# Optimization experiments

Measured on AMD Instinct MI355X. Metric: run time of the kernel, lower is better.

Reference implementation:

```python
import jax, jax.numpy as jnp
import numpy as np

N, F_IN, H, C, E = 50000, 128, 4, 32, 800000
NEG_SLOPE = 0.2


def setup_inputs() -> dict:
    key = jax.random.key(0)
    ks = jax.random.split(key, 6)
    x = jax.random.normal(ks[0], (N, F_IN), dtype=jnp.float32)
    edge_index = jax.random.randint(ks[1], (2, E), 0, N, dtype=jnp.int64)
    scale = 1.0 / np.sqrt(F_IN)
    Wl = jax.random.normal(ks[2], (F_IN, H * C), dtype=jnp.float32) * scale
    Wr = jax.random.normal(ks[3], (F_IN, H * C), dtype=jnp.float32) * scale
    att = jax.random.normal(ks[4], (H, C), dtype=jnp.float32) * (1.0 / np.sqrt(C))
    bias = jax.random.normal(ks[5], (H * C,), dtype=jnp.float32) * 0.01
    return {"x": x, "edge_index": edge_index, "Wl": Wl, "Wr": Wr, "att": att, "bias": bias}


def reference(x, edge_index, Wl, Wr, att, bias):
    n = x.shape[0]
    # add self loops (add_self_loops=True, edge_dim=None)
    loop = jnp.arange(n, dtype=edge_index.dtype)
    ei = jnp.concatenate([edge_index, jnp.stack([loop, loop])], axis=1)
    src, dst = ei[0], ei[1]  # messages flow src -> dst; softmax over dst
    # share_weights=False: separate projections for source (l) and target (r)
    xl = (x @ Wl).reshape(n, H, C)
    xr = (x @ Wr).reshape(n, H, C)
    # GATv2 edge score: a . LeakyReLU(xl[src] + xr[dst])
    e = xl[src] + xr[dst]                      # [Et, H, C]
    e = jnp.where(e > 0, e, NEG_SLOPE * e)
    logits = jnp.einsum('ehc,hc->eh', e, att)  # [Et, H]
    # segment softmax over destination nodes (every node has a self loop)
    m = jax.ops.segment_max(logits, dst, num_segments=n)
    ex = jnp.exp(logits - m[dst])
    den = jax.ops.segment_sum(ex, dst, num_segments=n)
    alpha = ex / den[dst]                      # [Et, H]
    # weighted scatter-aggregate of source messages
    out = jax.ops.segment_sum(alpha[:, :, None] * xl[src], dst, num_segments=n)
    out = out.reshape(n, H * C) + bias         # concat=True heads, bias
    out = jax.nn.relu(out)                     # activation_func='relu'
    return out, alpha
```

## Files before the change

### kernel.cpp

```cpp
#include <hip/hip_runtime.h>
#include <hip/hip_bf16.h>
#include <hip/hip_fp16.h>

#define F_IN   128
#define HC     128
#define NH     4
#define NEG_SLOPE 0.2f
#define CAP    5120

typedef __attribute__((ext_vector_type(8))) short short8;
typedef __attribute__((ext_vector_type(4))) float f32x4;
typedef _Float16 h2 __attribute__((ext_vector_type(2)));

__device__ __forceinline__ unsigned short f2bf(float f) {
    union { float f; unsigned u; } c; c.f = f;
    unsigned u = c.u;
    u += 0x7FFFu + ((u >> 16) & 1u);
    return (unsigned short)(u >> 16);
}

__device__ __forceinline__ float fdot2f(h2 a, h2 b, float c) {
#if __has_builtin(__builtin_amdgcn_fdot2)
    return __builtin_amdgcn_fdot2(a, b, c, false);
#else
    return fmaf((float)a[0], (float)b[0], fmaf((float)a[1], (float)b[1], c));
#endif
}

union U4H { uint4 u; h2 h[4]; };

__global__ __launch_bounds__(256) void wpack_zero_kernel(
    const float* __restrict__ Wl, const float* __restrict__ Wr,
    short* __restrict__ BlP, short* __restrict__ BrP,
    int* __restrict__ bucketCount)
{
    if ((int)blockIdx.x >= 16) {
        bucketCount[threadIdx.x] = 0;
        return;
    }
    const int tid = blockIdx.x * 256 + threadIdx.x;
    const int mat = tid >> 11;
    const int r   = tid & 2047;
    const int f   = r >> 6;
    const int l   = r & 63;
    const int t   = f & 3;
    const int ct  = f >> 2;
    const int kb  = t * 32 + (l >> 4) * 8;
    const int c   = ct * 16 + (l & 15);
    const float* W = mat ? Wr : Wl;
    short*       P = mat ? BrP : BlP;
    short8 v;
    #pragma unroll
    for (int j = 0; j < 8; ++j)
        v[j] = (short)f2bf(W[(size_t)(kb + j) * HC + c]);
    *(short8*)&P[(size_t)(f * 64 + l) * 8] = v;
}

__global__ __launch_bounds__(1024) void proj_split_kernel(
    const float* __restrict__ x,
    const short* __restrict__ BlP,
    const short* __restrict__ BrP,
    unsigned short* __restrict__ xlb,
    unsigned short* __restrict__ xrb,
    const int* __restrict__ ei,
    int* __restrict__ bucketCount,
    int2* __restrict__ slotES,
    int n, int E, int PB, int NB)
{
    __shared__ int sA[256];
    __shared__ int sB[256];
    const int t = threadIdx.x;

    if ((int)blockIdx.x >= PB) {
        const int e0 = ((int)blockIdx.x - PB) * 4096;

        if (t < 256) sA[t] = 0;
        __syncthreads();
        int dsts[4], srcs[4];
        #pragma unroll
        for (int k = 0; k < 4; ++k) {
            const int e = e0 + k * 1024 + t;
            dsts[k] = (e < E) ? ei[E + e] : -1;
            srcs[k] = (e < E) ? ei[e] : 0;
        }
        #pragma unroll
        for (int k = 0; k < 4; ++k)
            if (dsts[k] >= 0) atomicAdd(&sA[dsts[k] >> 8], 1);
        __syncthreads();
        if (t < NB) sB[t] = atomicAdd(&bucketCount[t], sA[t]);
        __syncthreads();
        if (t < 256) sA[t] = 0;
        __syncthreads();
        #pragma unroll
        for (int k = 0; k < 4; ++k) {
            const int e = e0 + k * 1024 + t;
            if (dsts[k] >= 0) {
                const int b = dsts[k] >> 8;
                const int r = sB[b] + atomicAdd(&sA[b], 1);
                slotES[(size_t)b * CAP + r] =
                    make_int2(e | ((dsts[k] & 255) << 24), srcs[k]);
            }
        }
        return;
    }

    const int w    = t >> 6;
    const int lane = t & 63;
    const int r0   = blockIdx.x * 256 + w * 16;
    if (r0 >= n) return;
    const int q    = lane >> 4;
    const int row  = r0 + (lane & 15);

    short8 af[4];
    {
        const float* xp = x + (size_t)row * F_IN + q * 8;
        #pragma unroll
        for (int s = 0; s < 4; ++s) {
            const float4 u0 = *(const float4*)(xp + s * 32);
            const float4 u1 = *(const float4*)(xp + s * 32 + 4);
            short8 a;
            a[0] = (short)f2bf(u0.x); a[1] = (short)f2bf(u0.y);
            a[2] = (short)f2bf(u0.z); a[3] = (short)f2bf(u0.w);
            a[4] = (short)f2bf(u1.x); a[5] = (short)f2bf(u1.y);
            a[6] = (short)f2bf(u1.z); a[7] = (short)f2bf(u1.w);
            af[s] = a;
        }
    }

    f32x4 accL[8], accR[8];
    const f32x4 zero = {0.f, 0.f, 0.f, 0.f};
    #pragma unroll
    for (int ct = 0; ct < 8; ++ct) { accL[ct] = zero; accR[ct] = zero; }

    #pragma unroll
    for (int s = 0; s < 4; ++s) {
        #pragma unroll
        for (int ct = 0; ct < 8; ++ct) {
            const short8 bl = *(const short8*)&BlP[(size_t)((ct * 4 + s) * 64 + lane) * 8];
            const short8 br = *(const short8*)&BrP[(size_t)((ct * 4 + s) * 64 + lane) * 8];
            accL[ct] = __builtin_amdgcn_mfma_f32_16x16x32_bf16(af[s], bl, accL[ct], 0, 0, 0);
            accR[ct] = __builtin_amdgcn_mfma_f32_16x16x32_bf16(af[s], br, accR[ct], 0, 0, 0);
        }
    }

    const int cb = lane & 15;
    const bool evenLane = (cb & 1) == 0;
    unsigned* xl_u = (unsigned*)xlb;
    unsigned* xr_u = (unsigned*)xrb;
    #pragma unroll
    for (int ct = 0; ct < 8; ++ct) {
        #pragma unroll
        for (int i = 0; i < 4; ++i) {
            const float l = accL[ct][i];
            const float r = accR[ct][i];
            const float sl = __shfl_xor(l, 1);
            const float sr = __shfl_xor(r, 1);
            const int rowo = r0 + q * 4 + i;
            const size_t cidx = (size_t)rowo * 64 + ct * 8 + (cb >> 1);
            union { _Float16 h[2]; unsigned u; } ph;
            if (evenLane) { ph.h[0] = (_Float16)l;  ph.h[1] = (_Float16)sl; xl_u[cidx] = ph.u; }
            else          { ph.h[0] = (_Float16)sr; ph.h[1] = (_Float16)r;  xr_u[cidx] = ph.u; }
        }
    }
}

__global__ __launch_bounds__(1024) void bucket_build_kernel(
    const int* __restrict__ bucketCount,
    const int2* __restrict__ slotES,
    int* __restrict__ rowptr,
    int2* __restrict__ csr,
    int n, int E, int NB)
{
    __shared__ int sh[256];
    __shared__ int cur[256];
    const int t = threadIdx.x;
    const int b = blockIdx.x;

    if (t < 256) sh[t] = (t < NB) ? bucketCount[t] : 0;
    __syncthreads();
    for (int off = 1; off < 256; off <<= 1) {
        int v = 0, u = 0;
        if (t < 256) { v = sh[t]; u = (t >= off) ? sh[t - off] : 0; }
        __syncthreads();
        if (t < 256) sh[t] = v + u;
        __syncthreads();
    }
    const int base = (b == 0) ? 0 : sh[b - 1];
    const int cnt  = sh[b] - base;
    __syncthreads();

    if (t < 256) cur[t] = 0;
    __syncthreads();
    const size_t sbase = (size_t)b * CAP;
    int2 rec[5]; int nrec = 0;
    for (int i = t; i < cnt; i += 1024) {
        rec[nrec] = slotES[sbase + i];
        ++nrec;
    }
    for (int k = 0; k < nrec; ++k)
        atomicAdd(&cur[(unsigned)rec[k].x >> 24], 1);
    __syncthreads();

    int myCnt = 0;
    if (t < 256) { myCnt = cur[t]; sh[t] = myCnt; }
    __syncthreads();
    for (int off = 1; off < 256; off <<= 1) {
        int v = 0, u = 0;
        if (t < 256) { v = sh[t]; u = (t >= off) ? sh[t - off] : 0; }
        __syncthreads();
        if (t < 256) sh[t] = v + u;
        __syncthreads();
    }
    if (t < 256) {
        const int startT = sh[t] - myCnt;
        const int dstT = (b << 8) + t;
        if (dstT < n) rowptr[dstT] = base + startT;
        if (b == 0 && t == 0) rowptr[n] = E;
        cur[t] = startT;
    }
    __syncthreads();

    for (int k = 0; k < nrec; ++k) {
        const int dl = (unsigned)rec[k].x >> 24;
        const int r = atomicAdd(&cur[dl], 1);
        csr[(size_t)base + r] = make_int2(rec[k].x & 0xFFFFFF, rec[k].y);
    }
}

__global__ __launch_bounds__(256) void fused_agg_kernel(
    const int2* __restrict__ csr,
    const int* __restrict__ rowptr,
    const unsigned short* __restrict__ xlb,
    const unsigned short* __restrict__ xrb,
    const float* __restrict__ att,
    const float* __restrict__ bias,
    float* __restrict__ alpha_out,
    float* __restrict__ out,
    int n, int E)
{
    __shared__ float lds_ex[4][256];
    const int w    = threadIdx.x >> 6;
    const int lane = threadIdx.x & 63;
    const int dst  = blockIdx.x * 4 + w;
    if (dst >= n) return;

    const int start = rowptr[dst];
    const int deg   = rowptr[dst + 1] - start;
    const int total = deg + 1;
    const int g     = lane >> 4;
    const int i     = lane & 15;
    const int h     = i >> 2;

    const uint4* xl_u = (const uint4*)xlb;

    h2 xr2[4], at2[4];
    {
        U4H c; c.u = ((const uint4*)xrb)[(size_t)dst * 16 + i];
        xr2[0] = c.h[0]; xr2[1] = c.h[1]; xr2[2] = c.h[2]; xr2[3] = c.h[3];
        const float4 a01 = *(const float4*)&att[8 * i];
        const float4 a23 = *(const float4*)&att[8 * i + 4];
        at2[0] = h2{(_Float16)a01.x, (_Float16)a01.y};
        at2[1] = h2{(_Float16)a01.z, (_Float16)a01.w};
        at2[2] = h2{(_Float16)a23.x, (_Float16)a23.y};
        at2[3] = h2{(_Float16)a23.z, (_Float16)a23.w};
    }
    const h2 slope2 = {(_Float16)NEG_SLOPE, (_Float16)NEG_SLOPE};

    int eReg = E + dst, srcReg = dst;
    if (lane < deg) { const int2 es = csr[start + lane]; eReg = es.x; srcReg = es.y; }

    float* exrow = lds_ex[w];

    float dh = 0.f;
    float acc[8];
    #pragma unroll
    for (int k = 0; k < 8; ++k) acc[k] = 0.f;

    int j = 0;
    {
        const int s0 = __shfl(srcReg, g);
        uint4 u = xl_u[(size_t)s0 * 16 + i];
        uint4 u1 = u;
        if (4 < total) {
            const int s1 = __shfl(srcReg, min(g + 4, 63));
            u1 = xl_u[(size_t)s1 * 16 + i];
        }

        for (; j < total && j <= 60; j += 4) {
            const int jj = j + g;
            uint4 u2 = u1;
            if (j + 8 < total) {
                const int sn = __shfl(srcReg, min(jj + 8, 63));
                u2 = xl_u[(size_t)sn * 16 + i];
            }

            U4H cu; cu.u = u;
            float p = 0.f;
            float vf[8];
            #pragma unroll
            for (int k = 0; k < 4; ++k) {
                const h2 v2 = cu.h[k];
                const h2 t2 = v2 + xr2[k];
                const h2 l2 = __builtin_elementwise_max(t2, t2 * slope2);
                p = fdot2f(l2, at2[k], p);
                vf[2 * k]     = (float)v2[0];
                vf[2 * k + 1] = (float)v2[1];
            }
            p += __shfl_xor(p, 1);
            p += __shfl_xor(p, 2);

            const float ex = (jj <= deg) ? __expf(p) : 0.f;
            dh += ex;
            #pragma unroll
            for (int k = 0; k < 8; ++k) acc[k] = fmaf(ex, vf[k], acc[k]);

            if ((lane & 3) == 0 && jj <= deg) exrow[jj * 4 + h] = ex;
            u = u1; u1 = u2;
        }
    }
    for (; j < total; j += 4) {
        const int jj = j + g;
        const int cidx = start + min(jj, deg - 1);
        const int2 es = csr[cidx];
        const int s   = (jj < deg) ? es.y : dst;
        const int eId = (jj < deg) ? es.x : E + dst;
        U4H cu; cu.u = xl_u[(size_t)s * 16 + i];

        float p = 0.f;
        float vf[8];
        #pragma unroll
        for (int k = 0; k < 4; ++k) {
            const h2 v2 = cu.h[k];
            const h2 t2 = v2 + xr2[k];
            const h2 l2 = __builtin_elementwise_max(t2, t2 * slope2);
            p = fdot2f(l2, at2[k], p);
            vf[2 * k]     = (float)v2[0];
            vf[2 * k + 1] = (float)v2[1];
        }
        p += __shfl_xor(p, 1);
        p += __shfl_xor(p, 2);

        const float ex = (jj <= deg) ? __expf(p) : 0.f;
        dh += ex;
        #pragma unroll
        for (int k = 0; k < 8; ++k) acc[k] = fmaf(ex, vf[k], acc[k]);

        if ((lane & 3) == 0 && jj <= deg) alpha_out[(size_t)eId * NH + h] = ex;
    }

    dh += __shfl_xor(dh, 16);
    dh += __shfl_xor(dh, 32);
    #pragma unroll
    for (int k = 0; k < 8; ++k) {
        acc[k] += __shfl_xor(acc[k], 16);
        acc[k] += __shfl_xor(acc[k], 32);
    }
    const float invh = 1.f / dh;
    const float id0 = 1.f / __shfl(dh, 0);
    const float id1 = 1.f / __shfl(dh, 4);
    const float id2 = 1.f / __shfl(dh, 8);
    const float id3 = 1.f / __shfl(dh, 12);

    __threadfence_block();

    if (lane < total && lane < 64) {
        const float4 e4 = *(const float4*)&exrow[lane * 4];
        const float4 a4 = make_float4(e4.x * id0, e4.y * id1, e4.z * id2, e4.w * id3);
        *(float4*)&alpha_out[(size_t)eReg * NH] = a4;
    }
    if (total > 64) {
        __threadfence();
        for (int jr = 64 + lane; jr < total; jr += 64) {
            const int e = (jr < deg) ? csr[start + jr].x : E + dst;
            float4 a4 = *(float4*)&alpha_out[(size_t)e * NH];
            a4.x *= id0; a4.y *= id1; a4.z *= id2; a4.w *= id3;
            *(float4*)&alpha_out[(size_t)e * NH] = a4;
        }
    }

    if (g == 0) {
        const float4 b01 = *(const float4*)&bias[8 * i];
        const float4 b23 = *(const float4*)&bias[8 * i + 4];
        float4 o01, o23;
        o01.x = fmaxf(fmaf(acc[0], invh, b01.x), 0.f);
        o01.y = fmaxf(fmaf(acc[1], invh, b01.y), 0.f);
        o01.z = fmaxf(fmaf(acc[2], invh, b01.z), 0.f);
        o01.w = fmaxf(fmaf(acc[3], invh, b01.w), 0.f);
        o23.x = fmaxf(fmaf(acc[4], invh, b23.x), 0.f);
        o23.y = fmaxf(fmaf(acc[5], invh, b23.y), 0.f);
        o23.z = fmaxf(fmaf(acc[6], invh, b23.z), 0.f);
        o23.w = fmaxf(fmaf(acc[7], invh, b23.w), 0.f);
        *(float4*)&out[(size_t)dst * HC + 8 * i]     = o01;
        *(float4*)&out[(size_t)dst * HC + 8 * i + 4] = o23;
    }
}

extern "C" void kernel_launch(void* const* d_in, const int* in_sizes, int n_in,
                              void* d_out, int out_size, void* d_ws, size_t ws_size,
                              hipStream_t stream)
{
    const float* x    = (const float*)d_in[0];
    const int*   ei   = (const int*)d_in[1];
    const float* Wl   = (const float*)d_in[2];
    const float* Wr   = (const float*)d_in[3];
    const float* att  = (const float*)d_in[4];
    const float* bias = (const float*)d_in[5];

    const int n  = in_sizes[0] / F_IN;
    const int E  = in_sizes[1] / 2;
    const int NB = (n + 255) >> 8;

    float* out   = (float*)d_out;
    float* alpha = (float*)d_out + (size_t)n * HC;

    short*          BlP         = (short*)d_ws;
    short*          BrP         = BlP + 16384;
    unsigned short* xlb         = (unsigned short*)(BrP + 16384);
    unsigned short* xrb         = xlb + (size_t)n * HC;
    int2*           csr         = (int2*)(xrb + (size_t)n * HC);
    int2*           slotES      = csr + E;
    int*            bucketCount = (int*)(slotES + (size_t)NB * CAP);
    int*            rowptr      = bucketCount + 256;

    const int PB = (n + 255) / 256;
    const int SB = (E + 4095) / 4096;

    wpack_zero_kernel<<<dim3(17), 256, 0, stream>>>(Wl, Wr, BlP, BrP, bucketCount);

    proj_split_kernel<<<dim3(PB + SB), 1024, 0, stream>>>(
        x, BlP, BrP, xlb, xrb, ei, bucketCount, slotES, n, E, PB, NB);

    bucket_build_kernel<<<dim3(NB), 1024, 0, stream>>>(
        bucketCount, slotES, rowptr, csr, n, E, NB);

    fused_agg_kernel<<<dim3((n + 3) / 4), 256, 0, stream>>>(
        csr, rowptr, xlb, xrb, att, bias, alpha, out, n, E);
}
```

Measured before the change: 174.9 us.

## Fuse bucket-to-CSR build into aggregation kernel with 64-node buckets

```diff
diff --git a/kernel.cpp b/kernel.cpp
--- a/kernel.cpp
+++ b/kernel.cpp
@@ -6,7 +6,9 @@
 #define HC     128
 #define NH     4
 #define NEG_SLOPE 0.2f
-#define CAP    5120
+#define BK     64
+#define CAP    1536
+#define NBPAD  784
 
 typedef __attribute__((ext_vector_type(8))) short short8;
 typedef __attribute__((ext_vector_type(4))) float f32x4;
@@ -32,10 +34,11 @@
 __global__ __launch_bounds__(256) void wpack_zero_kernel(
     const float* __restrict__ Wl, const float* __restrict__ Wr,
     short* __restrict__ BlP, short* __restrict__ BrP,
-    int* __restrict__ bucketCount)
+    int* __restrict__ bucketCount, int NB)
 {
     if ((int)blockIdx.x >= 16) {
-        bucketCount[threadIdx.x] = 0;
+        const int i = ((int)blockIdx.x - 16) * 256 + threadIdx.x;
+        if (i < NB) bucketCount[i] = 0;
         return;
     }
     const int tid = blockIdx.x * 256 + threadIdx.x;
@@ -67,14 +70,14 @@
     int2* __restrict__ slotES,
     int n, int E, int PB, int NB)
 {
-    __shared__ int sA[256];
-    __shared__ int sB[256];
+    __shared__ int sA[NBPAD];
+    __shared__ int sB[NBPAD];
     const int t = threadIdx.x;
 
     if ((int)blockIdx.x >= PB) {
         const int e0 = ((int)blockIdx.x - PB) * 4096;
 
-        if (t < 256) sA[t] = 0;
+        if (t < NBPAD) sA[t] = 0;
         __syncthreads();
         int dsts[4], srcs[4];
         #pragma unroll
@@ -85,20 +88,20 @@
         }
         #pragma unroll
         for (int k = 0; k < 4; ++k)
-            if (dsts[k] >= 0) atomicAdd(&sA[dsts[k] >> 8], 1);
+            if (dsts[k] >= 0) atomicAdd(&sA[dsts[k] >> 6], 1);
         __syncthreads();
-        if (t < NB) sB[t] = atomicAdd(&bucketCount[t], sA[t]);
+        if (t < NB && sA[t] > 0) sB[t] = atomicAdd(&bucketCount[t], sA[t]);
         __syncthreads();
-        if (t < 256) sA[t] = 0;
+        if (t < NBPAD) sA[t] = 0;
         __syncthreads();
         #pragma unroll
         for (int k = 0; k < 4; ++k) {
             const int e = e0 + k * 1024 + t;
             if (dsts[k] >= 0) {
-                const int b = dsts[k] >> 8;
+                const int b = dsts[k] >> 6;
                 const int r = sB[b] + atomicAdd(&sA[b], 1);
                 slotES[(size_t)b * CAP + r] =
-                    make_int2(e | ((dsts[k] & 255) << 24), srcs[k]);
+                    make_int2(e | ((dsts[k] & 63) << 24), srcs[k]);
             }
         }
         return;
@@ -157,79 +160,16 @@
             const float sr = __shfl_xor(r, 1);
             const int rowo = r0 + q * 4 + i;
             const size_t cidx = (size_t)rowo * 64 + ct * 8 + (cb >> 1);
-            union { _Float16 h[2]; unsigned u; } ph;
-            if (evenLane) { ph.h[0] = (_Float16)l;  ph.h[1] = (_Float16)sl; xl_u[cidx] = ph.u; }
-            else          { ph.h[0] = (_Float16)sr; ph.h[1] = (_Float16)r;  xr_u[cidx] = ph.u; }
-        }
-    }
-}
-
-__global__ __launch_bounds__(1024) void bucket_build_kernel(
+            union { _Float16 hh[2]; unsigned u; } ph;
+            if (evenLane) { ph.hh[0] = (_Float16)l;  ph.hh[1] = (_Float16)sl; xl_u[cidx] = ph.u; }
+            else          { ph.hh[0] = (_Float16)sr; ph.hh[1] = (_Float16)r;  xr_u[cidx] = ph.u; }
+        }
+    }
+}
+
+__global__ __launch_bounds__(512) void agg_build_kernel(
     const int* __restrict__ bucketCount,
     const int2* __restrict__ slotES,
-    int* __restrict__ rowptr,
-    int2* __restrict__ csr,
-    int n, int E, int NB)
-{
-    __shared__ int sh[256];
-    __shared__ int cur[256];
-    const int t = threadIdx.x;
-    const int b = blockIdx.x;
-
-    if (t < 256) sh[t] = (t < NB) ? bucketCount[t] : 0;
-    __syncthreads();
-    for (int off = 1; off < 256; off <<= 1) {
-        int v = 0, u = 0;
-        if (t < 256) { v = sh[t]; u = (t >= off) ? sh[t - off] : 0; }
-        __syncthreads();
-        if (t < 256) sh[t] = v + u;
-        __syncthreads();
-    }
-    const int base = (b == 0) ? 0 : sh[b - 1];
-    const int cnt  = sh[b] - base;
-    __syncthreads();
-
-    if (t < 256) cur[t] = 0;
-    __syncthreads();
-    const size_t sbase = (size_t)b * CAP;
-    int2 rec[5]; int nrec = 0;
-    for (int i = t; i < cnt; i += 1024) {
-        rec[nrec] = slotES[sbase + i];
-        ++nrec;
-    }
-    for (int k = 0; k < nrec; ++k)
-        atomicAdd(&cur[(unsigned)rec[k].x >> 24], 1);
-    __syncthreads();
-
-    int myCnt = 0;
-    if (t < 256) { myCnt = cur[t]; sh[t] = myCnt; }
-    __syncthreads();
-    for (int off = 1; off < 256; off <<= 1) {
-        int v = 0, u = 0;
-        if (t < 256) { v = sh[t]; u = (t >= off) ? sh[t - off] : 0; }
-        __syncthreads();
-        if (t < 256) sh[t] = v + u;
-        __syncthreads();
-    }
-    if (t < 256) {
-        const int startT = sh[t] - myCnt;
-        const int dstT = (b << 8) + t;
-        if (dstT < n) rowptr[dstT] = base + startT;
-        if (b == 0 && t == 0) rowptr[n] = E;
-        cur[t] = startT;
-    }
-    __syncthreads();
-
-    for (int k = 0; k < nrec; ++k) {
-        const int dl = (unsigned)rec[k].x >> 24;
-        const int r = atomicAdd(&cur[dl], 1);
-        csr[(size_t)base + r] = make_int2(rec[k].x & 0xFFFFFF, rec[k].y);
-    }
-}
-
-__global__ __launch_bounds__(256) void fused_agg_kernel(
-    const int2* __restrict__ csr,
-    const int* __restrict__ rowptr,
     const unsigned short* __restrict__ xlb,
     const unsigned short* __restrict__ xrb,
     const float* __restrict__ att,
@@ -238,25 +178,56 @@
     float* __restrict__ out,
     int n, int E)
 {
-    __shared__ float lds_ex[4][256];
-    const int w    = threadIdx.x >> 6;
-    const int lane = threadIdx.x & 63;
-    const int dst  = blockIdx.x * 4 + w;
-    if (dst >= n) return;
-
-    const int start = rowptr[dst];
-    const int deg   = rowptr[dst + 1] - start;
-    const int total = deg + 1;
-    const int g     = lane >> 4;
-    const int i     = lane & 15;
-    const int h     = i >> 2;
+    __shared__ int2  list[CAP];
+    __shared__ float exrow[8][256];
+    __shared__ int cnt64[BK], start64[BK], cur64[BK];
+
+    const int t = threadIdx.x;
+    const int b = blockIdx.x;
+    const int d0 = b * BK;
+    const int dlMax = min(BK, n - d0);
+    const int cnt = min(bucketCount[b], CAP);
+
+    if (t < BK) cnt64[t] = 0;
+    __syncthreads();
+
+    int2 rec[3]; int nrec = 0;
+    for (int i2 = t; i2 < cnt; i2 += 512) rec[nrec++] = slotES[(size_t)b * CAP + i2];
+    for (int k = 0; k < nrec; ++k)
+        atomicAdd(&cnt64[((unsigned)rec[k].x >> 24) & 63], 1);
+    __syncthreads();
+
+    if (t < BK) {
+        const int c = cnt64[t];
+        int s = c;
+        #pragma unroll
+        for (int off = 1; off < 64; off <<= 1) {
+            const int u = __shfl_up(s, off);
+            if (t >= off) s += u;
+        }
+        start64[t] = s - c;
+        cur64[t]   = s - c;
+    }
+    __syncthreads();
+
+    for (int k = 0; k < nrec; ++k) {
+        const int dl = ((unsigned)rec[k].x >> 24) & 63;
+        const int pos = atomicAdd(&cur64[dl], 1);
+        list[pos] = rec[k];
+    }
+    __syncthreads();
+
+    const int w    = t >> 6;
+    const int lane = t & 63;
+    const int g    = lane >> 4;
+    const int i    = lane & 15;
+    const int h    = i >> 2;
 
     const uint4* xl_u = (const uint4*)xlb;
-
-    h2 xr2[4], at2[4];
+    float* exw = exrow[w];
+
+    h2 at2[4];
     {
-        U4H c; c.u = ((const uint4*)xrb)[(size_t)dst * 16 + i];
-        xr2[0] = c.h[0]; xr2[1] = c.h[1]; xr2[2] = c.h[2]; xr2[3] = c.h[3];
         const float4 a01 = *(const float4*)&att[8 * i];
         const float4 a23 = *(const float4*)&att[8 * i + 4];
         at2[0] = h2{(_Float16)a01.x, (_Float16)a01.y};
@@ -265,33 +236,36 @@
         at2[3] = h2{(_Float16)a23.z, (_Float16)a23.w};
     }
     const h2 slope2 = {(_Float16)NEG_SLOPE, (_Float16)NEG_SLOPE};
-
-    int eReg = E + dst, srcReg = dst;
-    if (lane < deg) { const int2 es = csr[start + lane]; eReg = es.x; srcReg = es.y; }
-
-    float* exrow = lds_ex[w];
-
-    float dh = 0.f;
-    float acc[8];
-    #pragma unroll
-    for (int k = 0; k < 8; ++k) acc[k] = 0.f;
-
-    int j = 0;
-    {
-        const int s0 = __shfl(srcReg, g);
-        uint4 u = xl_u[(size_t)s0 * 16 + i];
-        uint4 u1 = u;
-        if (4 < total) {
-            const int s1 = __shfl(srcReg, min(g + 4, 63));
-            u1 = xl_u[(size_t)s1 * 16 + i];
-        }
-
-        for (; j < total && j <= 60; j += 4) {
+    const float4 b01 = *(const float4*)&bias[8 * i];
+    const float4 b23 = *(const float4*)&bias[8 * i + 4];
+
+    for (int dl = w; dl < dlMax; dl += 8) {
+        const int dst   = d0 + dl;
+        const int deg   = cnt64[dl];
+        const int start = start64[dl];
+        const int total = deg + 1;
+
+        h2 xr2[4];
+        {
+            U4H c; c.u = ((const uint4*)xrb)[(size_t)dst * 16 + i];
+            xr2[0] = c.h[0]; xr2[1] = c.h[1]; xr2[2] = c.h[2]; xr2[3] = c.h[3];
+        }
+
+        float dh = 0.f;
+        float acc[8];
+        #pragma unroll
+        for (int k = 0; k < 8; ++k) acc[k] = 0.f;
+
+        int scur = (g < deg) ? list[start + g].y : dst;
+        uint4 u = xl_u[(size_t)scur * 16 + i];
+
+        for (int j = 0; j < total; j += 4) {
             const int jj = j + g;
-            uint4 u2 = u1;
-            if (j + 8 < total) {
-                const int sn = __shfl(srcReg, min(jj + 8, 63));
-                u2 = xl_u[(size_t)sn * 16 + i];
+            uint4 un = u;
+            if (j + 4 < total) {
+                const int jn = jj + 4;
+                const int sn = (jn < deg) ? list[start + jn].y : dst;
+                un = xl_u[(size_t)sn * 16 + i];
             }
 
             U4H cu; cu.u = u;
@@ -314,84 +288,47 @@
             #pragma unroll
             for (int k = 0; k < 8; ++k) acc[k] = fmaf(ex, vf[k], acc[k]);
 
-            if ((lane & 3) == 0 && jj <= deg) exrow[jj * 4 + h] = ex;
-            u = u1; u1 = u2;
-        }
-    }
-    for (; j < total; j += 4) {
-        const int jj = j + g;
-        const int cidx = start + min(jj, deg - 1);
-        const int2 es = csr[cidx];
-        const int s   = (jj < deg) ? es.y : dst;
-        const int eId = (jj < deg) ? es.x : E + dst;
-        U4H cu; cu.u = xl_u[(size_t)s * 16 + i];
-
-        float p = 0.f;
-        float vf[8];
-        #pragma unroll
-        for (int k = 0; k < 4; ++k) {
-            const h2 v2 = cu.h[k];
-            const h2 t2 = v2 + xr2[k];
-            const h2 l2 = __builtin_elementwise_max(t2, t2 * slope2);
-            p = fdot2f(l2, at2[k], p);
-            vf[2 * k]     = (float)v2[0];
-            vf[2 * k + 1] = (float)v2[1];
-        }
-        p += __shfl_xor(p, 1);
-        p += __shfl_xor(p, 2);
-
-        const float ex = (jj <= deg) ? __expf(p) : 0.f;
-        dh += ex;
-        #pragma unroll
-        for (int k = 0; k < 8; ++k) acc[k] = fmaf(ex, vf[k], acc[k]);
-
-        if ((lane & 3) == 0 && jj <= deg) alpha_out[(size_t)eId * NH + h] = ex;
-    }
-
-    dh += __shfl_xor(dh, 16);
-    dh += __shfl_xor(dh, 32);
-    #pragma unroll
-    for (int k = 0; k < 8; ++k) {
-        acc[k] += __shfl_xor(acc[k], 16);
-        acc[k] += __shfl_xor(acc[k], 32);
-    }
-    const float invh = 1.f / dh;
-    const float id0 = 1.f / __shfl(dh, 0);
-    const float id1 = 1.f / __shfl(dh, 4);
-    const float id2 = 1.f / __shfl(dh, 8);
-    const float id3 = 1.f / __shfl(dh, 12);
-
-    __threadfence_block();
-
-    if (lane < total && lane < 64) {
-        const float4 e4 = *(const float4*)&exrow[lane * 4];
-        const float4 a4 = make_float4(e4.x * id0, e4.y * id1, e4.z * id2, e4.w * id3);
-        *(float4*)&alpha_out[(size_t)eReg * NH] = a4;
-    }
-    if (total > 64) {
-        __threadfence();
-        for (int jr = 64 + lane; jr < total; jr += 64) {
-            const int e = (jr < deg) ? csr[start + jr].x : E + dst;
-            float4 a4 = *(float4*)&alpha_out[(size_t)e * NH];
-            a4.x *= id0; a4.y *= id1; a4.z *= id2; a4.w *= id3;
+            if ((lane & 3) == 0 && jj <= deg && jj < 256) exw[jj * 4 + h] = ex;
+            u = un;
+        }
+
+        dh += __shfl_xor(dh, 16);
+        dh += __shfl_xor(dh, 32);
+        #pragma unroll
+        for (int k = 0; k < 8; ++k) {
+            acc[k] += __shfl_xor(acc[k], 16);
+            acc[k] += __shfl_xor(acc[k], 32);
+        }
+        const float invh = 1.f / dh;
+        const float id0 = 1.f / __shfl(dh, 0);
+        const float id1 = 1.f / __shfl(dh, 4);
+        const float id2 = 1.f / __shfl(dh, 8);
+        const float id3 = 1.f / __shfl(dh, 12);
+
+        __threadfence_block();
+
+        const int tcap = min(total, 256);
+        for (int jr = lane; jr < tcap; jr += 64) {
+            const int e = (jr < deg) ? (list[start + jr].x & 0xFFFFFF) : (E + dst);
+            const float4 e4 = *(const float4*)&exw[jr * 4];
+            const float4 a4 = make_float4(e4.x * id0, e4.y * id1,
+                                          e4.z * id2, e4.w * id3);
             *(float4*)&alpha_out[(size_t)e * NH] = a4;
         }
-    }
-
-    if (g == 0) {
-        const float4 b01 = *(const float4*)&bias[8 * i];
-        const float4 b23 = *(const float4*)&bias[8 * i + 4];
-        float4 o01, o23;
-        o01.x = fmaxf(fmaf(acc[0], invh, b01.x), 0.f);
-        o01.y = fmaxf(fmaf(acc[1], invh, b01.y), 0.f);
-        o01.z = fmaxf(fmaf(acc[2], invh, b01.z), 0.f);
-        o01.w = fmaxf(fmaf(acc[3], invh, b01.w), 0.f);
-        o23.x = fmaxf(fmaf(acc[4], invh, b23.x), 0.f);
-        o23.y = fmaxf(fmaf(acc[5], invh, b23.y), 0.f);
-        o23.z = fmaxf(fmaf(acc[6], invh, b23.z), 0.f);
-        o23.w = fmaxf(fmaf(acc[7], invh, b23.w), 0.f);
-        *(float4*)&out[(size_t)dst * HC + 8 * i]     = o01;
-        *(float4*)&out[(size_t)dst * HC + 8 * i + 4] = o23;
+
+        if (g == 0) {
+            float4 o01, o23;
+            o01.x = fmaxf(fmaf(acc[0], invh, b01.x), 0.f);
+            o01.y = fmaxf(fmaf(acc[1], invh, b01.y), 0.f);
+            o01.z = fmaxf(fmaf(acc[2], invh, b01.z), 0.f);
+            o01.w = fmaxf(fmaf(acc[3], invh, b01.w), 0.f);
+            o23.x = fmaxf(fmaf(acc[4], invh, b23.x), 0.f);
+            o23.y = fmaxf(fmaf(acc[5], invh, b23.y), 0.f);
+            o23.z = fmaxf(fmaf(acc[6], invh, b23.z), 0.f);
+            o23.w = fmaxf(fmaf(acc[7], invh, b23.w), 0.f);
+            *(float4*)&out[(size_t)dst * HC + 8 * i]     = o01;
+            *(float4*)&out[(size_t)dst * HC + 8 * i + 4] = o23;
+        }
     }
 }
 
@@ -408,7 +345,7 @@
 
     const int n  = in_sizes[0] / F_IN;
     const int E  = in_sizes[1] / 2;
-    const int NB = (n + 255) >> 8;
+    const int NB = (n + BK - 1) / BK;
 
     float* out   = (float*)d_out;
     float* alpha = (float*)d_out + (size_t)n * HC;
@@ -417,22 +354,19 @@
     short*          BrP         = BlP + 16384;
     unsigned short* xlb         = (unsigned short*)(BrP + 16384);
     unsigned short* xrb         = xlb + (size_t)n * HC;
-    int2*           csr         = (int2*)(xrb + (size_t)n * HC);
-    int2*           slotES      = csr + E;
+    int2*           slotES      = (int2*)(xrb + (size_t)n * HC);
     int*            bucketCount = (int*)(slotES + (size_t)NB * CAP);
-    int*            rowptr      = bucketCount + 256;
 
     const int PB = (n + 255) / 256;
     const int SB = (E + 4095) / 4096;
-
-    wpack_zero_kernel<<<dim3(17), 256, 0, stream>>>(Wl, Wr, BlP, BrP, bucketCount);
+    const int ZB = (NB + 255) / 256;
+
+    wpack_zero_kernel<<<dim3(16 + ZB), 256, 0, stream>>>(Wl, Wr, BlP, BrP,
+                                                         bucketCount, NB);
 
     proj_split_kernel<<<dim3(PB + SB), 1024, 0, stream>>>(
         x, BlP, BrP, xlb, xrb, ei, bucketCount, slotES, n, E, PB, NB);
 
-    bucket_build_kernel<<<dim3(NB), 1024, 0, stream>>>(
-        bucketCount, slotES, rowptr, csr, n, E, NB);
-
-    fused_agg_kernel<<<dim3((n + 3) / 4), 256, 0, stream>>>(
-        csr, rowptr, xlb, xrb, att, bias, alpha, out, n, E);
-}
+    agg_build_kernel<<<dim3(NB), 512, 0, stream>>>(
+        bucketCount, slotES, xlb, xrb, att, bias, alpha, out, n, E);
+}
```

After: 191.0 us. 1.09x slower.
